# Kernel optimization log

Hardware: AMD Instinct MI355X
Metric: run time of the kernel (lower is better)

Reference implementation:

```python
import jax, jax.numpy as jnp
import numpy as np

HEADS = 16
DIM_HEAD = 64


def setup_inputs() -> dict:
    key = jax.random.key(0)
    ks = jax.random.split(key, 5)
    b, n, dim = 4, 2048, 1024
    return {
        "x": jax.random.normal(ks[0], (b, n, dim), dtype=jnp.float32),
        "Wq": jax.random.normal(ks[1], (dim, HEADS * DIM_HEAD), dtype=jnp.float32) * (dim ** -0.5),
        "Wkv": jax.random.normal(ks[2], (dim, DIM_HEAD), dtype=jnp.float32) * (dim ** -0.5),
        "null_kv": jax.random.normal(ks[3], (DIM_HEAD,), dtype=jnp.float32),
        "Wout": jax.random.normal(ks[4], (HEADS * DIM_HEAD, dim), dtype=jnp.float32) * ((HEADS * DIM_HEAD) ** -0.5),
    }


def reference(x, Wq, Wkv, null_kv, Wout):
    b, n, dim = x.shape
    scale = DIM_HEAD ** -0.5
    # q: [b, h, n, d], pre-scaled
    q = (x @ Wq).reshape(b, n, HEADS, DIM_HEAD).transpose(0, 2, 1, 3) * scale
    # shared single-head kv: [b, n, d], prepend null token -> [b, n+1, d]
    kv = x @ Wkv
    kv = jnp.concatenate([jnp.broadcast_to(null_kv, (b, 1, DIM_HEAD)), kv], axis=1)
    # sim: [b, h, n, n+1]
    sim = jnp.einsum('bhid,bjd->bhij', q, kv)
    mask_value = -jnp.finfo(sim.dtype).max
    # causal: query i may attend kv cols 0..i+1 (null at col 0)
    i, j = sim.shape[-2], sim.shape[-1]
    causal_mask = jnp.triu(jnp.ones((i, j), dtype=bool), k=j - i + 1)
    sim = jnp.where(causal_mask, mask_value, sim)
    attn = jax.nn.softmax(sim.astype(jnp.float32), axis=-1)
    out = jnp.einsum('bhij,bjd->bhid', attn, kv.astype(jnp.float32))
    out = out.transpose(0, 2, 1, 3).reshape(b, n, HEADS * DIM_HEAD)
    return out @ Wout
```

## Files before the change

### kernel.cpp

```cpp
#include <hip/hip_runtime.h>
#include <hip/hip_bf16.h>

#define HEADS  16
#define DHEAD  64
#define BATCH  4
#define SEQ    2048
#define DIM    1024
#define KVROWS 2112
#define CSHIFT 24.0f

typedef __hip_bfloat16 bf16;
typedef __attribute__((ext_vector_type(8))) short s8v;
typedef __attribute__((ext_vector_type(4))) short s4v;
typedef __attribute__((ext_vector_type(4))) float f4v;

__device__ __forceinline__ void gl_lds16(const void* g, void* l) {
  __builtin_amdgcn_global_load_lds(
      (const __attribute__((address_space(1))) unsigned int*)g,
      (__attribute__((address_space(3))) unsigned int*)l, 16, 0, 0);
}

__global__ void convert_kernel(const float* __restrict__ in, bf16* __restrict__ out) {
  const size_t i = ((size_t)blockIdx.x * 256 + threadIdx.x) * 8;
  const float4 a = *(const float4*)&in[i];
  const float4 b = *(const float4*)&in[i + 4];
  bf16 v[8] = {__float2bfloat16(a.x), __float2bfloat16(a.y),
               __float2bfloat16(a.z), __float2bfloat16(a.w),
               __float2bfloat16(b.x), __float2bfloat16(b.y),
               __float2bfloat16(b.z), __float2bfloat16(b.w)};
  *(s8v*)&out[i] = *(s8v*)v;
}

__global__ void transpose_kernel(const float* __restrict__ in, bf16* __restrict__ out,
                                 int R, int C) {
  __shared__ bf16 tile[32][33];
  const int c0 = blockIdx.x * 32, r0 = blockIdx.y * 32;
  const int tx = threadIdx.x, ty = threadIdx.y;
#pragma unroll
  for (int i = 0; i < 32; i += 8)
    tile[ty + i][tx] = __float2bfloat16(in[(size_t)(r0 + ty + i) * C + c0 + tx]);
  __syncthreads();
#pragma unroll
  for (int i = 0; i < 32; i += 8)
    out[(size_t)(c0 + ty + i) * R + r0 + tx] = tile[tx][ty + i];
}

template <typename OT>
__global__ __launch_bounds__(256) void gemm_async_kernel(
    const bf16* __restrict__ A, const bf16* __restrict__ BT,
    OT* __restrict__ C, int K, int c_ld, float alpha) {
  __shared__ bf16 As[128 * 32];
  __shared__ bf16 Bs[128 * 32];
  const int m0 = blockIdx.x * 128, n0 = blockIdx.y * 128;
  const int t = threadIdx.x;
  const int w = t >> 6, l = t & 63, lr = l & 15, lq = l >> 4;
  const int wm = (w & 1) * 64, wn = (w >> 1) * 64;
  f4v acc[4][4] = {};

  const int rowl = l >> 2;
  const int cl = ((l & 3) ^ ((l >> 3) & 3)) * 8;
  const bf16* gA0 = A  + (size_t)(m0 + 32 * w + rowl) * K + cl;
  const bf16* gA1 = A  + (size_t)(m0 + 32 * w + 16 + rowl) * K + cl;
  const bf16* gB0 = BT + (size_t)(n0 + 32 * w + rowl) * K + cl;
  const bf16* gB1 = BT + (size_t)(n0 + 32 * w + 16 + rowl) * K + cl;
  bf16* lA0 = As + (2 * w) * 512;
  bf16* lA1 = As + (2 * w + 1) * 512;
  bf16* lB0 = Bs + (2 * w) * 512;
  bf16* lB1 = Bs + (2 * w + 1) * 512;

  const int sw = lq ^ ((lr >> 1) & 3);
  const s8v* As16 = (const s8v*)As;
  const s8v* Bs16 = (const s8v*)Bs;

  for (int k0 = 0; k0 < K; k0 += 32) {
    __syncthreads();
    gl_lds16(gA0 + k0, lA0);
    gl_lds16(gA1 + k0, lA1);
    gl_lds16(gB0 + k0, lB0);
    gl_lds16(gB1 + k0, lB1);
    __syncthreads();
    s8v a[4], b[4];
#pragma unroll
    for (int mt = 0; mt < 4; mt++) a[mt] = As16[(wm + mt * 16 + lr) * 4 + sw];
#pragma unroll
    for (int ct = 0; ct < 4; ct++) b[ct] = Bs16[(wn + ct * 16 + lr) * 4 + sw];
#pragma unroll
    for (int mt = 0; mt < 4; mt++)
#pragma unroll
      for (int ct = 0; ct < 4; ct++)
        acc[mt][ct] = __builtin_amdgcn_mfma_f32_16x16x32_bf16(a[mt], b[ct], acc[mt][ct], 0, 0, 0);
  }
#pragma unroll
  for (int mt = 0; mt < 4; mt++)
#pragma unroll
    for (int ct = 0; ct < 4; ct++)
#pragma unroll
      for (int r = 0; r < 4; r++) {
        const int row = m0 + wm + mt * 16 + lq * 4 + r;
        const int col = n0 + wn + ct * 16 + lr;
        const float v = acc[mt][ct][r] * alpha;
        if constexpr (__is_same(OT, float)) C[(size_t)row * c_ld + col] = v;
        else                                C[(size_t)row * c_ld + col] = __float2bfloat16(v);
      }
}

__global__ __launch_bounds__(256) void gemm_kv_kernel(
    const bf16* __restrict__ A, const bf16* __restrict__ BT,
    bf16* __restrict__ kvbuf, bf16* __restrict__ kvbufT, int K) {
  __shared__ bf16 As[128][32];
  __shared__ bf16 Bs[64][32];
  const int m0 = blockIdx.x * 128;
  const int t = threadIdx.x;
  const int w = t >> 6, l = t & 63, lr = l & 15, lq = l >> 4;
  f4v acc[2][4] = {};
  const int arow = t >> 1, acol = (t & 1) * 16;
  const int brow = t >> 2, bcol = (t & 3) * 8;

  for (int k0 = 0; k0 < K; k0 += 32) {
    __syncthreads();
    *(s8v*)&As[arow][acol]     = *(const s8v*)&A[(size_t)(m0 + arow) * K + k0 + acol];
    *(s8v*)&As[arow][acol + 8] = *(const s8v*)&A[(size_t)(m0 + arow) * K + k0 + acol + 8];
    *(s8v*)&Bs[brow][bcol]     = *(const s8v*)&BT[(size_t)brow * K + k0 + bcol];
    __syncthreads();
    s8v a0 = *(const s8v*)&As[w * 32 + lr][lq * 8];
    s8v a1 = *(const s8v*)&As[w * 32 + 16 + lr][lq * 8];
#pragma unroll
    for (int ct = 0; ct < 4; ct++) {
      s8v bf = *(const s8v*)&Bs[ct * 16 + lr][lq * 8];
      acc[0][ct] = __builtin_amdgcn_mfma_f32_16x16x32_bf16(a0, bf, acc[0][ct], 0, 0, 0);
      acc[1][ct] = __builtin_amdgcn_mfma_f32_16x16x32_bf16(a1, bf, acc[1][ct], 0, 0, 0);
    }
  }
#pragma unroll
  for (int mt = 0; mt < 2; mt++)
#pragma unroll
    for (int ct = 0; ct < 4; ct++)
#pragma unroll
      for (int r = 0; r < 4; r++) {
        const int m = m0 + w * 32 + mt * 16 + lq * 4 + r;
        const int col = ct * 16 + lr;
        const int bb = m >> 11, jj = (m & 2047) + 1;
        const bf16 v = __float2bfloat16(acc[mt][ct][r]);
        kvbuf [(size_t)(bb * KVROWS + jj) * DHEAD + col] = v;
        kvbufT[(size_t)(bb * DHEAD + col) * KVROWS + jj] = v;
      }
}

__global__ void fill_null_tail_kernel(const float* __restrict__ null_kv,
                                      bf16* __restrict__ kvbuf,
                                      bf16* __restrict__ kvbufT) {
  const int idx = blockIdx.x * 256 + threadIdx.x;
  const int d = idx & 63;
  const int s = (idx >> 6) & 63;
  const int b = idx >> 12;
  const int row = (s == 0) ? 0 : 2048 + s;
  const bf16 v = (s == 0) ? __float2bfloat16(null_kv[d]) : __float2bfloat16(0.f);
  kvbuf [(size_t)(b * KVROWS + row) * DHEAD + d] = v;
  kvbufT[(size_t)(b * DHEAD + d) * KVROWS + row] = v;
}

__global__ __launch_bounds__(256) void attn_kernel(
    const bf16* __restrict__ q,
    const bf16* __restrict__ kv,
    const bf16* __restrict__ kvT,
    bf16* __restrict__ o) {
  __shared__ bf16 kvs [64][68];
  __shared__ bf16 kvsT[64][68];
  __shared__ bf16 Ps[4][16][68];
  const int t = threadIdx.x, w = t >> 6, l = t & 63, lr = l & 15, lq = l >> 4;
  const int blk = blockIdx.x;
  const int qt = 31 - (blk >> 5);
  const int rem = blk & 31, hp = rem >> 2, b = rem & 3;
  const int q0 = qt * 64;
  const int iw = q0 + w * 16 + lr;

  const bf16* qbase = q + ((size_t)(b * SEQ) + iw) * DIM + hp * 128;
  s8v qb[2][2];
#pragma unroll
  for (int hh = 0; hh < 2; hh++) {
    qb[hh][0] = *(const s8v*)&qbase[hh * 64 + lq * 8];
    qb[hh][1] = *(const s8v*)&qbase[hh * 64 + 32 + lq * 8];
  }

  f4v oaccT[2][4] = {};
  float l_lane[2] = {0.f, 0.f};
  const bf16* kvb  = kv  + (size_t)b * KVROWS * DHEAD;
  const bf16* kvTb = kvT + (size_t)b * DHEAD * KVROWS;
  const int jend = q0 + 65;
  const int srow = t >> 2, scol = (t & 3) * 16;

  s8v rkv0 = *(const s8v*)&kvb[(size_t)srow * DHEAD + scol];
  s8v rkv1 = *(const s8v*)&kvb[(size_t)srow * DHEAD + scol + 8];
  s8v rkT0 = *(const s8v*)&kvTb[(size_t)srow * KVROWS + scol];
  s8v rkT1 = *(const s8v*)&kvTb[(size_t)srow * KVROWS + scol + 8];

  for (int j0 = 0; j0 < jend; j0 += 64) {
    __syncthreads();
    *(s8v*)&kvs[srow][scol]      = rkv0;
    *(s8v*)&kvs[srow][scol + 8]  = rkv1;
    *(s8v*)&kvsT[srow][scol]     = rkT0;
    *(s8v*)&kvsT[srow][scol + 8] = rkT1;
    __syncthreads();

    const int jn = min(j0 + 64, KVROWS - 64);
    rkv0 = *(const s8v*)&kvb[(size_t)(jn + srow) * DHEAD + scol];
    rkv1 = *(const s8v*)&kvb[(size_t)(jn + srow) * DHEAD + scol + 8];
    rkT0 = *(const s8v*)&kvTb[(size_t)srow * KVROWS + jn + scol];
    rkT1 = *(const s8v*)&kvTb[(size_t)srow * KVROWS + jn + scol + 8];

    f4v st[2][4];
#pragma unroll
    for (int jt = 0; jt < 4; jt++) {
      s8v a0 = *(const s8v*)&kvs[jt * 16 + lr][lq * 8];
      s8v a1 = *(const s8v*)&kvs[jt * 16 + lr][32 + lq * 8];
#pragma unroll
      for (int hh = 0; hh < 2; hh++) {
        f4v z = {-CSHIFT, -CSHIFT, -CSHIFT, -CSHIFT};
        z = __builtin_amdgcn_mfma_f32_16x16x32_bf16(a0, qb[hh][0], z, 0, 0, 0);
        z = __builtin_amdgcn_mfma_f32_16x16x32_bf16(a1, qb[hh][1], z, 0, 0, 0);
        st[hh][jt] = z;
      }
    }

    const bool diag = (j0 + 62 > q0 + w * 16);
#pragma unroll
    for (int hh = 0; hh < 2; hh++) {
      if (diag) {
#pragma unroll
        for (int jt = 0; jt < 4; jt++)
#pragma unroll
          for (int r = 0; r < 4; r++) {
            const int jg = j0 + jt * 16 + lq * 4 + r;
            if (jg > iw + 1) st[hh][jt][r] = -1e30f;
          }
      }
      float rs = 0.f;
#pragma unroll
      for (int jt = 0; jt < 4; jt++)
#pragma unroll
        for (int r = 0; r < 4; r++) {
          const float pv = exp2f(st[hh][jt][r]);
          st[hh][jt][r] = pv;
          rs += pv;
        }
      l_lane[hh] += rs;

#pragma unroll
      for (int jt = 0; jt < 4; jt++) {
        s4v pk;
#pragma unroll
        for (int r = 0; r < 4; r++) {
          bf16 h16 = __float2bfloat16(st[hh][jt][r]);
          pk[r] = *(short*)&h16;
        }
        *(s4v*)&Ps[w][lr][jt * 16 + lq * 4] = pk;
      }
      const s8v pb0 = *(const s8v*)&Ps[w][lr][lq * 8];
      const s8v pb1 = *(const s8v*)&Ps[w][lr][32 + lq * 8];
#pragma unroll
      for (int dt = 0; dt < 4; dt++) {
        s8v a0 = *(const s8v*)&kvsT[dt * 16 + lr][lq * 8];
        s8v a1 = *(const s8v*)&kvsT[dt * 16 + lr][32 + lq * 8];
        oaccT[hh][dt] = __builtin_amdgcn_mfma_f32_16x16x32_bf16(a0, pb0, oaccT[hh][dt], 0, 0, 0);
        oaccT[hh][dt] = __builtin_amdgcn_mfma_f32_16x16x32_bf16(a1, pb1, oaccT[hh][dt], 0, 0, 0);
      }
    }
  }

#pragma unroll
  for (int hh = 0; hh < 2; hh++) {
    float lt = l_lane[hh];
    lt += __shfl_xor(lt, 16);
    lt += __shfl_xor(lt, 32);
    const float inv = 1.0f / lt;
#pragma unroll
    for (int dt = 0; dt < 4; dt++) {
      s4v pk;
#pragma unroll
      for (int r = 0; r < 4; r++) {
        bf16 h16 = __float2bfloat16(oaccT[hh][dt][r] * inv);
        pk[r] = *(short*)&h16;
      }
      *(s4v*)&Ps[w][lr][dt * 16 + lq * 4] = pk;
    }
    const int orow = l >> 2, od = (l & 3) * 16;
    s8v o0 = *(const s8v*)&Ps[w][orow][od];
    s8v o1 = *(const s8v*)&Ps[w][orow][od + 8];
    bf16* op = o + ((size_t)(b * SEQ) + q0 + w * 16 + orow) * DIM + hp * 128 + hh * 64 + od;
    *(s8v*)&op[0] = o0;
    *(s8v*)&op[8] = o1;
  }
}

extern "C" void kernel_launch(void* const* d_in, const int* in_sizes, int n_in,
                              void* d_out, int out_size, void* d_ws, size_t ws_size,
                              hipStream_t stream) {
  const float* x       = (const float*)d_in[0];
  const float* Wq      = (const float*)d_in[1];
  const float* Wkv     = (const float*)d_in[2];
  const float* null_kv = (const float*)d_in[3];
  const float* Wout    = (const float*)d_in[4];
  float* out = (float*)d_out;

  char* dob = (char*)d_out;
  bf16* q      = (bf16*)dob;
  bf16* kvbufT = (bf16*)(dob + (size_t)16 * 1024 * 1024);
  char* p = (char*)d_ws;
  bf16* att   = (bf16*)p;
  bf16* xb    = (bf16*)(p + (size_t)16 * 1024 * 1024);
  bf16* WoutT = (bf16*)(p + (size_t)32 * 1024 * 1024);
  bf16* kvbuf = (bf16*)(p + (size_t)34 * 1024 * 1024);
  bf16* WqT   = att;
  bf16* WkvT  = att + (size_t)DIM * DIM;

  convert_kernel<<<(BATCH * SEQ * DIM) / (256 * 8), 256, 0, stream>>>(x, xb);

  const dim3 tb(32, 8);
  transpose_kernel<<<dim3(32, 32), tb, 0, stream>>>(Wq,   WqT,   DIM, DIM);
  transpose_kernel<<<dim3(2, 32),  tb, 0, stream>>>(Wkv,  WkvT,  DIM, DHEAD);
  transpose_kernel<<<dim3(32, 32), tb, 0, stream>>>(Wout, WoutT, DIM, DIM);

  gemm_async_kernel<bf16><<<dim3(64, 8), 256, 0, stream>>>(xb, WqT, q, DIM, DIM,
                                                           0.125f * 1.44269504089f);
  gemm_kv_kernel<<<64, 256, 0, stream>>>(xb, WkvT, kvbuf, kvbufT, DIM);
  fill_null_tail_kernel<<<(BATCH * 64 * 64) / 256, 256, 0, stream>>>(null_kv, kvbuf, kvbufT);

  attn_kernel<<<32 * 8 * BATCH, 256, 0, stream>>>(q, kvbuf, kvbufT, att);

  gemm_async_kernel<float><<<dim3(64, 8), 256, 0, stream>>>(att, WoutT, out, DIM, DIM, 1.0f);
}
```

Baseline: 248.2 us.

## Pair causal query tiles per block, double-buffer KV, keep P in registers

The attention kernel now processes two query tiles per block (tile 31-pi and tile pi) so causal work is balanced, halving the grid. K/V tiles are double-buffered in LDS with a one-tile-ahead register prefetch, removing one barrier per iteration. The P matrix is repacked in registers with permlane swaps instead of round-tripping through LDS, and the row sum is computed by an MFMA against a ones vector. setprio hints are added around the MFMA sections. Risks include the larger LDS footprint and fewer blocks, which may reduce occupancy or latency hiding.

```diff
diff --git a/kernel.cpp b/kernel.cpp
--- a/kernel.cpp
+++ b/kernel.cpp
@@ -13,11 +13,23 @@
 typedef __attribute__((ext_vector_type(8))) short s8v;
 typedef __attribute__((ext_vector_type(4))) short s4v;
 typedef __attribute__((ext_vector_type(4))) float f4v;
+typedef __attribute__((ext_vector_type(4))) unsigned int u32x4;
 
 __device__ __forceinline__ void gl_lds16(const void* g, void* l) {
   __builtin_amdgcn_global_load_lds(
       (const __attribute__((address_space(1))) unsigned int*)g,
       (__attribute__((address_space(3))) unsigned int*)l, 16, 0, 0);
+}
+
+__device__ __forceinline__ unsigned pk2(float lo, float hi) {
+  bf16 x = __float2bfloat16(lo), y = __float2bfloat16(hi);
+  return (unsigned)*(unsigned short*)&x | ((unsigned)*(unsigned short*)&y << 16);
+}
+__device__ __forceinline__ void plswap32(unsigned &a, unsigned &b) {
+  asm("v_permlane32_swap_b32 %0, %1" : "+v"(a), "+v"(b));
+}
+__device__ __forceinline__ void plswap16(unsigned &a, unsigned &b) {
+  asm("v_permlane16_swap_b32 %0, %1" : "+v"(a), "+v"(b));
 }
 
 __global__ void convert_kernel(const float* __restrict__ in, bf16* __restrict__ out) {
@@ -164,132 +176,160 @@
     const bf16* __restrict__ kv,
     const bf16* __restrict__ kvT,
     bf16* __restrict__ o) {
-  __shared__ bf16 kvs [64][68];
-  __shared__ bf16 kvsT[64][68];
+  __shared__ bf16 kvs [2][64][68];
+  __shared__ bf16 kvsT[2][64][68];
   __shared__ bf16 Ps[4][16][68];
   const int t = threadIdx.x, w = t >> 6, l = t & 63, lr = l & 15, lq = l >> 4;
   const int blk = blockIdx.x;
-  const int qt = 31 - (blk >> 5);
+  const int pi = blk >> 5;
   const int rem = blk & 31, hp = rem >> 2, b = rem & 3;
-  const int q0 = qt * 64;
-  const int iw = q0 + w * 16 + lr;
-
-  const bf16* qbase = q + ((size_t)(b * SEQ) + iw) * DIM + hp * 128;
-  s8v qb[2][2];
-#pragma unroll
-  for (int hh = 0; hh < 2; hh++) {
-    qb[hh][0] = *(const s8v*)&qbase[hh * 64 + lq * 8];
-    qb[hh][1] = *(const s8v*)&qbase[hh * 64 + 32 + lq * 8];
-  }
-
-  f4v oaccT[2][4] = {};
-  float l_lane[2] = {0.f, 0.f};
+
   const bf16* kvb  = kv  + (size_t)b * KVROWS * DHEAD;
   const bf16* kvTb = kvT + (size_t)b * DHEAD * KVROWS;
-  const int jend = q0 + 65;
   const int srow = t >> 2, scol = (t & 3) * 16;
-
-  s8v rkv0 = *(const s8v*)&kvb[(size_t)srow * DHEAD + scol];
-  s8v rkv1 = *(const s8v*)&kvb[(size_t)srow * DHEAD + scol + 8];
-  s8v rkT0 = *(const s8v*)&kvTb[(size_t)srow * KVROWS + scol];
-  s8v rkT1 = *(const s8v*)&kvTb[(size_t)srow * KVROWS + scol + 8];
-
-  for (int j0 = 0; j0 < jend; j0 += 64) {
-    __syncthreads();
-    *(s8v*)&kvs[srow][scol]      = rkv0;
-    *(s8v*)&kvs[srow][scol + 8]  = rkv1;
-    *(s8v*)&kvsT[srow][scol]     = rkT0;
-    *(s8v*)&kvsT[srow][scol + 8] = rkT1;
-    __syncthreads();
-
-    const int jn = min(j0 + 64, KVROWS - 64);
-    rkv0 = *(const s8v*)&kvb[(size_t)(jn + srow) * DHEAD + scol];
-    rkv1 = *(const s8v*)&kvb[(size_t)(jn + srow) * DHEAD + scol + 8];
-    rkT0 = *(const s8v*)&kvTb[(size_t)srow * KVROWS + jn + scol];
-    rkT1 = *(const s8v*)&kvTb[(size_t)srow * KVROWS + jn + scol + 8];
-
-    f4v st[2][4];
-#pragma unroll
-    for (int jt = 0; jt < 4; jt++) {
-      s8v a0 = *(const s8v*)&kvs[jt * 16 + lr][lq * 8];
-      s8v a1 = *(const s8v*)&kvs[jt * 16 + lr][32 + lq * 8];
+  const short onebf = (short)0x3F80;
+  const s8v ones = {onebf, onebf, onebf, onebf, onebf, onebf, onebf, onebf};
+
+  s8v rkv0, rkv1, rkT0, rkT1;
+#define LOADKV(jr)                                                              \
+  do {                                                                          \
+    rkv0 = *(const s8v*)&kvb[(size_t)((jr) + srow) * DHEAD + scol];             \
+    rkv1 = *(const s8v*)&kvb[(size_t)((jr) + srow) * DHEAD + scol + 8];         \
+    rkT0 = *(const s8v*)&kvTb[(size_t)srow * KVROWS + (jr) + scol];             \
+    rkT1 = *(const s8v*)&kvTb[(size_t)srow * KVROWS + (jr) + scol + 8];         \
+  } while (0)
+#define STAGE(bi)                                                               \
+  do {                                                                          \
+    *(s8v*)&kvs[bi][srow][scol]      = rkv0;                                    \
+    *(s8v*)&kvs[bi][srow][scol + 8]  = rkv1;                                    \
+    *(s8v*)&kvsT[bi][srow][scol]     = rkT0;                                    \
+    *(s8v*)&kvsT[bi][srow][scol + 8] = rkT1;                                    \
+  } while (0)
+
+  for (int seg = 0; seg < 2; ++seg) {
+    const int qt = seg ? pi : 31 - pi;
+    const int q0 = qt * 64;
+    const int iw = q0 + w * 16 + lr;
+    const int jend = q0 + 65;
+
+    const bf16* qbase = q + ((size_t)(b * SEQ) + iw) * DIM + hp * 128;
+    s8v qb[2][2];
+#pragma unroll
+    for (int hh = 0; hh < 2; hh++) {
+      qb[hh][0] = *(const s8v*)&qbase[hh * 64 + lq * 8];
+      qb[hh][1] = *(const s8v*)&qbase[hh * 64 + 32 + lq * 8];
+    }
+
+    f4v oaccT[2][4] = {};
+    f4v lacc[2] = {};
+
+    __syncthreads();
+    LOADKV(0);
+    STAGE(0);
+    LOADKV(64);
+    int cur = 0;
+
+    for (int j0 = 0; j0 < jend; j0 += 64) {
+      __syncthreads();
+      STAGE(cur ^ 1);
+      LOADKV(min(j0 + 128, KVROWS - 64));
+
+      f4v st[2][4];
+      __builtin_amdgcn_s_setprio(1);
+#pragma unroll
+      for (int jt = 0; jt < 4; jt++) {
+        s8v a0 = *(const s8v*)&kvs[cur][jt * 16 + lr][lq * 8];
+        s8v a1 = *(const s8v*)&kvs[cur][jt * 16 + lr][32 + lq * 8];
+#pragma unroll
+        for (int hh = 0; hh < 2; hh++) {
+          f4v z = {-CSHIFT, -CSHIFT, -CSHIFT, -CSHIFT};
+          z = __builtin_amdgcn_mfma_f32_16x16x32_bf16(a0, qb[hh][0], z, 0, 0, 0);
+          z = __builtin_amdgcn_mfma_f32_16x16x32_bf16(a1, qb[hh][1], z, 0, 0, 0);
+          st[hh][jt] = z;
+        }
+      }
+      __builtin_amdgcn_s_setprio(0);
+
+      const bool diag = (j0 + 62 > q0 + w * 16);
+      s8v pb[2][2];
 #pragma unroll
       for (int hh = 0; hh < 2; hh++) {
-        f4v z = {-CSHIFT, -CSHIFT, -CSHIFT, -CSHIFT};
-        z = __builtin_amdgcn_mfma_f32_16x16x32_bf16(a0, qb[hh][0], z, 0, 0, 0);
-        z = __builtin_amdgcn_mfma_f32_16x16x32_bf16(a1, qb[hh][1], z, 0, 0, 0);
-        st[hh][jt] = z;
-      }
+        if (diag) {
+#pragma unroll
+          for (int jt = 0; jt < 4; jt++)
+#pragma unroll
+            for (int r = 0; r < 4; r++) {
+              const int jg = j0 + jt * 16 + lq * 4 + r;
+              if (jg > iw + 1) st[hh][jt][r] = -1e30f;
+            }
+        }
+#pragma unroll
+        for (int jt = 0; jt < 4; jt++)
+#pragma unroll
+          for (int r = 0; r < 4; r++)
+            st[hh][jt][r] = exp2f(st[hh][jt][r]);
+
+        unsigned w00 = pk2(st[hh][0][0], st[hh][0][1]);
+        unsigned w01 = pk2(st[hh][0][2], st[hh][0][3]);
+        unsigned w10 = pk2(st[hh][1][0], st[hh][1][1]);
+        unsigned w11 = pk2(st[hh][1][2], st[hh][1][3]);
+        unsigned w20 = pk2(st[hh][2][0], st[hh][2][1]);
+        unsigned w21 = pk2(st[hh][2][2], st[hh][2][3]);
+        unsigned w30 = pk2(st[hh][3][0], st[hh][3][1]);
+        unsigned w31 = pk2(st[hh][3][2], st[hh][3][3]);
+        plswap32(w00, w10); plswap16(w00, w10);
+        plswap32(w01, w11); plswap16(w01, w11);
+        plswap32(w20, w30); plswap16(w20, w30);
+        plswap32(w21, w31); plswap16(w21, w31);
+        u32x4 p0 = {w00, w01, w10, w11};
+        u32x4 p1 = {w20, w21, w30, w31};
+        pb[hh][0] = __builtin_bit_cast(s8v, p0);
+        pb[hh][1] = __builtin_bit_cast(s8v, p1);
+      }
+
+      __builtin_amdgcn_s_setprio(1);
+#pragma unroll
+      for (int hh = 0; hh < 2; hh++) {
+        lacc[hh] = __builtin_amdgcn_mfma_f32_16x16x32_bf16(ones, pb[hh][0], lacc[hh], 0, 0, 0);
+        lacc[hh] = __builtin_amdgcn_mfma_f32_16x16x32_bf16(ones, pb[hh][1], lacc[hh], 0, 0, 0);
+      }
+#pragma unroll
+      for (int dt = 0; dt < 4; dt++) {
+        s8v a0 = *(const s8v*)&kvsT[cur][dt * 16 + lr][lq * 8];
+        s8v a1 = *(const s8v*)&kvsT[cur][dt * 16 + lr][32 + lq * 8];
+#pragma unroll
+        for (int hh = 0; hh < 2; hh++) {
+          oaccT[hh][dt] = __builtin_amdgcn_mfma_f32_16x16x32_bf16(a0, pb[hh][0], oaccT[hh][dt], 0, 0, 0);
+          oaccT[hh][dt] = __builtin_amdgcn_mfma_f32_16x16x32_bf16(a1, pb[hh][1], oaccT[hh][dt], 0, 0, 0);
+        }
+      }
+      __builtin_amdgcn_s_setprio(0);
+      cur ^= 1;
     }
 
-    const bool diag = (j0 + 62 > q0 + w * 16);
 #pragma unroll
     for (int hh = 0; hh < 2; hh++) {
-      if (diag) {
-#pragma unroll
-        for (int jt = 0; jt < 4; jt++)
-#pragma unroll
-          for (int r = 0; r < 4; r++) {
-            const int jg = j0 + jt * 16 + lq * 4 + r;
-            if (jg > iw + 1) st[hh][jt][r] = -1e30f;
-          }
-      }
-      float rs = 0.f;
-#pragma unroll
-      for (int jt = 0; jt < 4; jt++)
+      const float inv = 1.0f / lacc[hh][0];
+#pragma unroll
+      for (int dt = 0; dt < 4; dt++) {
+        s4v pk;
 #pragma unroll
         for (int r = 0; r < 4; r++) {
-          const float pv = exp2f(st[hh][jt][r]);
-          st[hh][jt][r] = pv;
-          rs += pv;
-        }
-      l_lane[hh] += rs;
-
-#pragma unroll
-      for (int jt = 0; jt < 4; jt++) {
-        s4v pk;
-#pragma unroll
-        for (int r = 0; r < 4; r++) {
-          bf16 h16 = __float2bfloat16(st[hh][jt][r]);
+          bf16 h16 = __float2bfloat16(oaccT[hh][dt][r] * inv);
           pk[r] = *(short*)&h16;
         }
-        *(s4v*)&Ps[w][lr][jt * 16 + lq * 4] = pk;
-      }
-      const s8v pb0 = *(const s8v*)&Ps[w][lr][lq * 8];
-      const s8v pb1 = *(const s8v*)&Ps[w][lr][32 + lq * 8];
-#pragma unroll
-      for (int dt = 0; dt < 4; dt++) {
-        s8v a0 = *(const s8v*)&kvsT[dt * 16 + lr][lq * 8];
-        s8v a1 = *(const s8v*)&kvsT[dt * 16 + lr][32 + lq * 8];
-        oaccT[hh][dt] = __builtin_amdgcn_mfma_f32_16x16x32_bf16(a0, pb0, oaccT[hh][dt], 0, 0, 0);
-        oaccT[hh][dt] = __builtin_amdgcn_mfma_f32_16x16x32_bf16(a1, pb1, oaccT[hh][dt], 0, 0, 0);
-      }
+        *(s4v*)&Ps[w][lr][dt * 16 + lq * 4] = pk;
+      }
+      const int orow = l >> 2, od = (l & 3) * 16;
+      s8v o0 = *(const s8v*)&Ps[w][orow][od];
+      s8v o1 = *(const s8v*)&Ps[w][orow][od + 8];
+      bf16* op = o + ((size_t)(b * SEQ) + q0 + w * 16 + orow) * DIM + hp * 128 + hh * 64 + od;
+      *(s8v*)&op[0] = o0;
+      *(s8v*)&op[8] = o1;
     }
   }
-
-#pragma unroll
-  for (int hh = 0; hh < 2; hh++) {
-    float lt = l_lane[hh];
-    lt += __shfl_xor(lt, 16);
-    lt += __shfl_xor(lt, 32);
-    const float inv = 1.0f / lt;
-#pragma unroll
-    for (int dt = 0; dt < 4; dt++) {
-      s4v pk;
-#pragma unroll
-      for (int r = 0; r < 4; r++) {
-        bf16 h16 = __float2bfloat16(oaccT[hh][dt][r] * inv);
-        pk[r] = *(short*)&h16;
-      }
-      *(s4v*)&Ps[w][lr][dt * 16 + lq * 4] = pk;
-    }
-    const int orow = l >> 2, od = (l & 3) * 16;
-    s8v o0 = *(const s8v*)&Ps[w][orow][od];
-    s8v o1 = *(const s8v*)&Ps[w][orow][od + 8];
-    bf16* op = o + ((size_t)(b * SEQ) + q0 + w * 16 + orow) * DIM + hp * 128 + hh * 64 + od;
-    *(s8v*)&op[0] = o0;
-    *(s8v*)&op[8] = o1;
-  }
+#undef LOADKV
+#undef STAGE
 }
 
 extern "C" void kernel_launch(void* const* d_in, const int* in_sizes, int n_in,
@@ -325,7 +365,7 @@
   gemm_kv_kernel<<<64, 256, 0, stream>>>(xb, WkvT, kvbuf, kvbufT, DIM);
   fill_null_tail_kernel<<<(BATCH * 64 * 64) / 256, 256, 0, stream>>>(null_kv, kvbuf, kvbufT);
 
-  attn_kernel<<<32 * 8 * BATCH, 256, 0, stream>>>(q, kvbuf, kvbufT, att);
+  attn_kernel<<<16 * 8 * BATCH, 256, 0, stream>>>(q, kvbuf, kvbufT, att);
 
   gemm_async_kernel<float><<<dim3(64, 8), 256, 0, stream>>>(att, WoutT, out, DIM, DIM, 1.0f);
 }
```

New measurement: 260.3 us. 1.05x slower.

## Compute softmax row sums via ones-MFMA and hoist kvT loads across heads

Applied to the files above, without the earlier changes.

Replaces the per-lane scalar accumulation of exponentials plus end-of-loop shuffles with an MFMA against a ones vector, so the row sum comes out of the matrix unit on bf16-rounded probabilities. The PV product is restructured to load each kvT fragment once and reuse it for both heads, and s_setprio hints are placed around the MFMA blocks. This trades VALU adds for extra MFMA issue and slightly changes the normaliser, which now uses bf16-rounded P.

```diff
diff --git a/kernel.cpp b/kernel.cpp
--- a/kernel.cpp
+++ b/kernel.cpp
@@ -183,7 +183,10 @@
   }
 
   f4v oaccT[2][4] = {};
-  float l_lane[2] = {0.f, 0.f};
+  f4v lacc[2] = {};
+  const short onebf = (short)0x3F80;
+  const s8v ones = {onebf, onebf, onebf, onebf, onebf, onebf, onebf, onebf};
+
   const bf16* kvb  = kv  + (size_t)b * KVROWS * DHEAD;
   const bf16* kvTb = kvT + (size_t)b * DHEAD * KVROWS;
   const int jend = q0 + 65;
@@ -209,6 +212,7 @@
     rkT1 = *(const s8v*)&kvTb[(size_t)srow * KVROWS + jn + scol + 8];
 
     f4v st[2][4];
+    __builtin_amdgcn_s_setprio(1);
 #pragma unroll
     for (int jt = 0; jt < 4; jt++) {
       s8v a0 = *(const s8v*)&kvs[jt * 16 + lr][lq * 8];
@@ -221,8 +225,10 @@
         st[hh][jt] = z;
       }
     }
+    __builtin_amdgcn_s_setprio(0);
 
     const bool diag = (j0 + 62 > q0 + w * 16);
+    s8v pb[2][2];
 #pragma unroll
     for (int hh = 0; hh < 2; hh++) {
       if (diag) {
@@ -234,16 +240,11 @@
             if (jg > iw + 1) st[hh][jt][r] = -1e30f;
           }
       }
-      float rs = 0.f;
 #pragma unroll
       for (int jt = 0; jt < 4; jt++)
 #pragma unroll
-        for (int r = 0; r < 4; r++) {
-          const float pv = exp2f(st[hh][jt][r]);
-          st[hh][jt][r] = pv;
-          rs += pv;
-        }
-      l_lane[hh] += rs;
+        for (int r = 0; r < 4; r++)
+          st[hh][jt][r] = exp2f(st[hh][jt][r]);
 
 #pragma unroll
       for (int jt = 0; jt < 4; jt++) {
@@ -255,24 +256,32 @@
         }
         *(s4v*)&Ps[w][lr][jt * 16 + lq * 4] = pk;
       }
-      const s8v pb0 = *(const s8v*)&Ps[w][lr][lq * 8];
-      const s8v pb1 = *(const s8v*)&Ps[w][lr][32 + lq * 8];
-#pragma unroll
-      for (int dt = 0; dt < 4; dt++) {
-        s8v a0 = *(const s8v*)&kvsT[dt * 16 + lr][lq * 8];
-        s8v a1 = *(const s8v*)&kvsT[dt * 16 + lr][32 + lq * 8];
-        oaccT[hh][dt] = __builtin_amdgcn_mfma_f32_16x16x32_bf16(a0, pb0, oaccT[hh][dt], 0, 0, 0);
-        oaccT[hh][dt] = __builtin_amdgcn_mfma_f32_16x16x32_bf16(a1, pb1, oaccT[hh][dt], 0, 0, 0);
-      }
-    }
+      pb[hh][0] = *(const s8v*)&Ps[w][lr][lq * 8];
+      pb[hh][1] = *(const s8v*)&Ps[w][lr][32 + lq * 8];
+    }
+
+    __builtin_amdgcn_s_setprio(1);
+#pragma unroll
+    for (int hh = 0; hh < 2; hh++) {
+      lacc[hh] = __builtin_amdgcn_mfma_f32_16x16x32_bf16(ones, pb[hh][0], lacc[hh], 0, 0, 0);
+      lacc[hh] = __builtin_amdgcn_mfma_f32_16x16x32_bf16(ones, pb[hh][1], lacc[hh], 0, 0, 0);
+    }
+#pragma unroll
+    for (int dt = 0; dt < 4; dt++) {
+      s8v a0 = *(const s8v*)&kvsT[dt * 16 + lr][lq * 8];
+      s8v a1 = *(const s8v*)&kvsT[dt * 16 + lr][32 + lq * 8];
+#pragma unroll
+      for (int hh = 0; hh < 2; hh++) {
+        oaccT[hh][dt] = __builtin_amdgcn_mfma_f32_16x16x32_bf16(a0, pb[hh][0], oaccT[hh][dt], 0, 0, 0);
+        oaccT[hh][dt] = __builtin_amdgcn_mfma_f32_16x16x32_bf16(a1, pb[hh][1], oaccT[hh][dt], 0, 0, 0);
+      }
+    }
+    __builtin_amdgcn_s_setprio(0);
   }
 
 #pragma unroll
   for (int hh = 0; hh < 2; hh++) {
-    float lt = l_lane[hh];
-    lt += __shfl_xor(lt, 16);
-    lt += __shfl_xor(lt, 32);
-    const float inv = 1.0f / lt;
+    const float inv = 1.0f / lacc[hh][0];
 #pragma unroll
     for (int dt = 0; dt < 4; dt++) {
       s4v pk;
```

After: 255.5 us. 2.9% more time.
